# Performance work log

Hardware: AMD Instinct MI355X
Metric: run time of the kernel (lower is better)

Reference implementation:

```python
import jax, jax.numpy as jnp
import numpy as np

HIDDEN = 1024
HEADS = 16
HEAD_DIM = HIDDEN // HEADS
SCALE = HEAD_DIM ** -0.5
NEG_INF = float(-2 ** 32 + 1)


def setup_inputs() -> dict:
    key = jax.random.key(0)
    ks = jax.random.split(key, 10)
    B, N = 8, 1024
    std = HIDDEN ** -0.5
    inp = {
        "query": jax.random.normal(ks[0], (B, N, HIDDEN), dtype=jnp.float32),
        "mask": jax.random.randint(ks[1], (B, N), 0, 2, dtype=jnp.int32),
        "Wq": jax.random.normal(ks[2], (HIDDEN, HIDDEN), dtype=jnp.float32) * std,
        "bq": jnp.zeros((HIDDEN,), dtype=jnp.float32),
        "Wk": jax.random.normal(ks[3], (HIDDEN, HIDDEN), dtype=jnp.float32) * std,
        "bk": jnp.zeros((HIDDEN,), dtype=jnp.float32),
        "Wv": jax.random.normal(ks[4], (HIDDEN, HIDDEN), dtype=jnp.float32) * std,
        "bv": jnp.zeros((HIDDEN,), dtype=jnp.float32),
        "Wo": jax.random.normal(ks[5], (HIDDEN, HIDDEN), dtype=jnp.float32) * std,
        "bo": jnp.zeros((HIDDEN,), dtype=jnp.float32),
    }
    return inp


def reference(query, mask, Wq, bq, Wk, bk, Wv, bv, Wo, bo):
    B, N, C = query.shape
    H, D = HEADS, HEAD_DIM
    # projections: [B,N,C] -> [B,H,N,D]
    q = (query @ Wq + bq).reshape(B, N, H, D).transpose(0, 2, 1, 3)
    k = (query @ Wk + bk).reshape(B, N, H, D).transpose(0, 2, 1, 3)
    v = (query @ Wv + bv).reshape(B, N, H, D).transpose(0, 2, 1, 3)
    # scores [B,H,N,S]
    attn = jnp.einsum("bhnd,bhsd->bhns", q, k) * SCALE
    # padding mask broadcast over query positions: mask [B,S] -> [B,1,1,S]
    m = mask[:, None, None, :]
    attn = jnp.where(m == 0, jnp.float32(NEG_INF), attn)
    attn = jax.nn.softmax(attn, axis=-1)
    out = jnp.einsum("bhns,bhsd->bhnd", attn, v)
    out = out.transpose(0, 2, 1, 3).reshape(B, N, C)
    out = out @ Wo + bo
    return out
```

## Files before the change

### kernel.cpp

```cpp
#include <hip/hip_runtime.h>
#include <hip/hip_bf16.h>

typedef __bf16 bf16x8 __attribute__((ext_vector_type(8)));
typedef float f32x4 __attribute__((ext_vector_type(4)));
typedef float f32x16 __attribute__((ext_vector_type(16)));
typedef int i32x2 __attribute__((ext_vector_type(2)));
typedef __hip_bfloat16 bf16;

#define QK_SCALE 0.1803368801111204f

__device__ __forceinline__ f32x4 mfma_bf16(bf16x8 a, bf16x8 b, f32x4 c) {
  return __builtin_amdgcn_mfma_f32_16x16x32_bf16(a, b, c, 0, 0, 0);
}
__device__ __forceinline__ f32x16 mfma32(bf16x8 a, bf16x8 b, f32x16 c) {
  return __builtin_amdgcn_mfma_f32_32x32x16_bf16(a, b, c, 0, 0, 0);
}

__device__ __forceinline__ void gload16(const void* g, void* l) {
  __builtin_amdgcn_global_load_lds(
      (const __attribute__((address_space(1))) void*)g,
      (__attribute__((address_space(3))) void*)l, 16, 0, 0);
}

__global__ void cvt_bf16_kernel(const float* __restrict__ in, bf16* __restrict__ out) {
  int i = (blockIdx.x * 256 + threadIdx.x) * 4;
  float4 v = *reinterpret_cast<const float4*>(in + i);
  union { bf16 h[4]; uint2 u; } t;
  t.h[0] = __float2bfloat16(v.x);
  t.h[1] = __float2bfloat16(v.y);
  t.h[2] = __float2bfloat16(v.z);
  t.h[3] = __float2bfloat16(v.w);
  *reinterpret_cast<uint2*>(out + i) = t.u;
}

__global__ void transpose_w_kernel(const float* __restrict__ Wq, const float* __restrict__ Wk,
                                   const float* __restrict__ Wv, const float* __restrict__ Wo,
                                   bf16* __restrict__ Wqkv_t, bf16* __restrict__ Wot) {
  __shared__ float tile[32][33];
  int z = blockIdx.z;
  const float* src = (z == 0) ? Wq : (z == 1) ? Wk : (z == 2) ? Wv : Wo;
  bf16* dst = (z < 3) ? (Wqkv_t + (size_t)z * 1048576) : Wot;
  int tx = threadIdx.x, ty = threadIdx.y;
  int c0 = blockIdx.x * 32, r0 = blockIdx.y * 32;
#pragma unroll
  for (int i = 0; i < 32; i += 8)
    tile[ty + i][tx] = src[(r0 + ty + i) * 1024 + c0 + tx];
  __syncthreads();
#pragma unroll
  for (int i = 0; i < 32; i += 8)
    dst[(c0 + ty + i) * 1024 + r0 + tx] = __float2bfloat16(tile[tx][ty + i]);
}

__global__ __launch_bounds__(256) void gemm_qkv_kernel(
    const bf16* __restrict__ A, const bf16* __restrict__ Bt,
    const float* __restrict__ bq, const float* __restrict__ bk, const float* __restrict__ bv,
    bf16* __restrict__ Qb, bf16* __restrict__ Kb, bf16* __restrict__ Vt) {
  __shared__ __align__(16) bf16 As[2][128 * 32];
  __shared__ __align__(16) bf16 Bs[2][128 * 32];
  const int K = 1024;
  const int TILES_N = 24;
  const int NWG = 1536, CPX = NWG / 8;
  int bid0 = blockIdx.x;
  int bid = (bid0 % 8) * CPX + bid0 / 8;
  int bm = bid / TILES_N, bn = bid % TILES_N;
  int t = threadIdx.x;
  int lane = t & 63, w = t >> 6;
  int fr = lane & 15, fk = (lane >> 4) * 8;
  int wr = w >> 1, wc = w & 1;
  int srow = t >> 2, scol = (t & 3) * 8;

  const bf16* Ablk = A + (size_t)(bm * 128) * K;
  const bf16* Bblk = Bt + (size_t)(bn * 128) * K;

  auto stage = [&](int bufi, int k0) {
    char* ad = (char*)As[bufi] + t * 16;
    char* bd = (char*)Bs[bufi] + t * 16;
    gload16(Ablk + (size_t)srow * K + k0 + scol, ad);
    gload16(Ablk + (size_t)(srow + 64) * K + k0 + scol, ad + 4096);
    gload16(Bblk + (size_t)srow * K + k0 + scol, bd);
    gload16(Bblk + (size_t)(srow + 64) * K + k0 + scol, bd + 4096);
  };

  f32x4 acc[4][4] = {};

  stage(0, 0);
  __syncthreads();

  for (int k0 = 0; k0 < K; k0 += 32) {
    int cur = (k0 >> 5) & 1;
    if (k0 + 32 < K) stage(cur ^ 1, k0 + 32);
    bf16x8 a[4], b[4];
#pragma unroll
    for (int m = 0; m < 4; m++) a[m] = *(const bf16x8*)&As[cur][(wr * 64 + m * 16 + fr) * 32 + fk];
#pragma unroll
    for (int n = 0; n < 4; n++) b[n] = *(const bf16x8*)&Bs[cur][(wc * 64 + n * 16 + fr) * 32 + fk];
#pragma unroll
    for (int m = 0; m < 4; m++)
#pragma unroll
      for (int n = 0; n < 4; n++)
        acc[m][n] = mfma_bf16(a[m], b[n], acc[m][n]);
    __syncthreads();
  }

  int sel = (bn * 128) >> 10;
  const float* bias = (sel == 0) ? bq : (sel == 1) ? bk : bv;
#pragma unroll
  for (int m = 0; m < 4; m++) {
#pragma unroll
    for (int n = 0; n < 4; n++) {
      f32x4 c = acc[m][n];
      if (sel == 2) {
        int grow0 = bm * 128 + wr * 64 + m * 16 + (lane >> 4) * 4;
        int gcol = bn * 128 + wc * 64 + n * 16 + fr;
        int cc = gcol & 1023;
        int bb = grow0 >> 10, nr0 = grow0 & 1023;
        int h = cc >> 6, d = cc & 63;
        union { bf16 h4[4]; uint2 u; } o;
#pragma unroll
        for (int j = 0; j < 4; j++) o.h4[j] = __float2bfloat16(c[j] + bias[cc]);
        *(uint2*)&Vt[((size_t)(bb * 16 + h) * 64 + d) * 1024 + nr0] = o.u;
      } else {
#pragma unroll
        for (int j = 0; j < 4; j++) {
          int grow = bm * 128 + wr * 64 + m * 16 + (lane >> 4) * 4 + j;
          int gcol = bn * 128 + wc * 64 + n * 16 + fr;
          int cc = gcol & 1023;
          float val = c[j] + bias[cc];
          int bb = grow >> 10, nr = grow & 1023;
          int h = cc >> 6, d = cc & 63;
          int bh = bb * 16 + h;
          if (sel == 0) {
            Qb[((size_t)bh * 1024 + nr) * 64 + d] = __float2bfloat16(val * QK_SCALE);
          } else {
            Kb[((size_t)bh * 1024 + nr) * 64 + d] = __float2bfloat16(val);
          }
        }
      }
    }
  }
}

__global__ __launch_bounds__(256) void attn_kernel(
    const bf16* __restrict__ Qb, const bf16* __restrict__ Kb, const bf16* __restrict__ Vt,
    const int* __restrict__ mask, bf16* __restrict__ AO) {
  __shared__ unsigned pmw[32][2][8];
  __shared__ __align__(16) bf16 Ks[2][4096];
  __shared__ __align__(16) bf16 Vs[2][4096];

  int bid = blockIdx.x;
  int logical = (bid & 7) * 128 + (bid >> 3);
  int bh = logical >> 3;
  int qt = logical & 7;
  int b = bh >> 4, h = bh & 15;
  int t = threadIdx.x, w = t >> 6, lane = t & 63;
  int ql = lane & 31, hi = lane >> 5, hi8 = hi * 8;

#pragma unroll
  for (int rep = 0; rep < 2; rep++) {
    int idx = t + rep * 256;
    int T = idx >> 4, hh = (idx >> 3) & 1, i = idx & 7;
    int k0 = T * 32 + hh * 4 + 2 * (i & 1) + 8 * (i >> 1);
    unsigned lo = mask[b * 1024 + k0] ? 0xFFFFu : 0u;
    unsigned hg = mask[b * 1024 + k0 + 1] ? 0xFFFF0000u : 0u;
    pmw[T][hh][i] = lo | hg;
  }

  const bf16* Qh = Qb + (size_t)bh * 65536;
  const bf16* Kh = Kb + (size_t)bh * 65536;
  const bf16* Vh = Vt + (size_t)bh * 65536;

  int r0 = t >> 3;
  int sc = (t & 7) ^ (r0 & 7);

  auto stage = [&](int bufi, int kt) {
    char* kd = (char*)Ks[bufi] + t * 16;
    char* vd = (char*)Vs[bufi] + t * 16;
    gload16(Kh + (size_t)(kt + r0) * 64 + sc * 8, kd);
    gload16(Kh + (size_t)(kt + r0 + 32) * 64 + sc * 8, kd + 4096);
    gload16(Vh + (size_t)r0 * 1024 + kt + sc * 8, vd);
    gload16(Vh + (size_t)(r0 + 32) * 1024 + kt + sc * 8, vd + 4096);
  };

  int qn = qt * 128 + w * 32;
  bf16x8 qf[4];
#pragma unroll
  for (int c = 0; c < 4; c++)
    qf[c] = *(const bf16x8*)&Qh[(qn + ql) * 64 + c * 16 + hi8];

  bf16x8 ones;
#pragma unroll
  for (int j = 0; j < 8; j++) ones[j] = (__bf16)1.0f;

  f32x16 accO0 = {}, accO1 = {}, accL = {};
  float mrow = -3.0e38f;

  stage(0, 0);
  __syncthreads();

  for (int kt = 0; kt < 1024; kt += 64) {
    int cur = (kt >> 6) & 1;
    if (kt + 64 < 1024) stage(cur ^ 1, kt + 64);
    const char* Kc = (const char*)Ks[cur];
    const char* Vc = (const char*)Vs[cur];

#pragma unroll
    for (int sub = 0; sub < 2; sub++) {
      int Ti = (kt >> 5) + sub;

      int krow = sub * 32 + ql;
      int ksw = (krow & 7) << 4;
      f32x16 s = {};
#pragma unroll
      for (int c = 0; c < 4; c++) {
        bf16x8 kf = *(const bf16x8*)(Kc + krow * 128 + ((c * 32 + hi * 16) ^ ksw));
        s = mfma32(kf, qf[c], s);
      }

      float m0 = fmaxf(fmaxf(s[0], s[1]), s[2]);
      float m1 = fmaxf(fmaxf(s[3], s[4]), s[5]);
      float m2 = fmaxf(fmaxf(s[6], s[7]), s[8]);
      float m3 = fmaxf(fmaxf(s[9], s[10]), s[11]);
      float m4 = fmaxf(fmaxf(s[12], s[13]), s[14]);
      float pm = fmaxf(fmaxf(fmaxf(m0, m1), m2), fmaxf(fmaxf(m3, m4), s[15]));
      pm = fmaxf(pm, __shfl_xor(pm, 32));

      if (!__all(pm - mrow <= 8.0f)) {
        float mnew = fmaxf(mrow, pm);
        float corr = __builtin_amdgcn_exp2f(mrow - mnew);
        accL[0] *= corr;
#pragma unroll
        for (int r = 0; r < 16; r++) { accO0[r] *= corr; accO1[r] *= corr; }
        mrow = mnew;
      }

#pragma unroll
      for (int r = 0; r < 16; r++) s[r] = __builtin_amdgcn_exp2f(s[r] - mrow);
      uint4 mwa = *(const uint4*)&pmw[Ti][hi][0];
      uint4 mwb = *(const uint4*)&pmw[Ti][hi][4];
      unsigned wds[8];
#pragma unroll
      for (int i = 0; i < 8; i++) {
        union { bf16 q[2]; unsigned u; } pk_;
        pk_.q[0] = __float2bfloat16(s[2 * i]);
        pk_.q[1] = __float2bfloat16(s[2 * i + 1]);
        wds[i] = pk_.u;
      }
      wds[0] &= mwa.x; wds[1] &= mwa.y; wds[2] &= mwa.z; wds[3] &= mwa.w;
      wds[4] &= mwb.x; wds[5] &= mwb.y; wds[6] &= mwb.z; wds[7] &= mwb.w;

      i32x2 r02 = __builtin_amdgcn_permlane32_swap((int)wds[0], (int)wds[2], false, false);
      i32x2 r13 = __builtin_amdgcn_permlane32_swap((int)wds[1], (int)wds[3], false, false);
      i32x2 r46 = __builtin_amdgcn_permlane32_swap((int)wds[4], (int)wds[6], false, false);
      i32x2 r57 = __builtin_amdgcn_permlane32_swap((int)wds[5], (int)wds[7], false, false);
      union { int i[4]; bf16x8 v; } y0, y1;
      y0.i[0] = r02[0]; y0.i[1] = r13[0]; y0.i[2] = r02[1]; y0.i[3] = r13[1];
      y1.i[0] = r46[0]; y1.i[1] = r57[0]; y1.i[2] = r46[1]; y1.i[3] = r57[1];

      int vr0 = ql, vr1 = 32 + ql;
      int vs0 = (vr0 & 7) << 4, vs1 = (vr1 & 7) << 4;
      bf16x8 vc0 = *(const bf16x8*)(Vc + vr0 * 128 + ((sub * 64 + hi * 16) ^ vs0));
      bf16x8 vc1 = *(const bf16x8*)(Vc + vr0 * 128 + ((sub * 64 + 32 + hi * 16) ^ vs0));
      bf16x8 vc2 = *(const bf16x8*)(Vc + vr1 * 128 + ((sub * 64 + hi * 16) ^ vs1));
      bf16x8 vc3 = *(const bf16x8*)(Vc + vr1 * 128 + ((sub * 64 + 32 + hi * 16) ^ vs1));
      accO0 = mfma32(vc0, y0.v, accO0);
      accO0 = mfma32(vc1, y1.v, accO0);
      accO1 = mfma32(vc2, y0.v, accO1);
      accO1 = mfma32(vc3, y1.v, accO1);
      accL = mfma32(ones, y0.v, accL);
      accL = mfma32(ones, y1.v, accL);
    }
    __syncthreads();
  }

  float rl = 1.0f / accL[0];
  size_t rowbase = ((size_t)(b * 1024 + qn + ql)) * 1024 + h * 64;
#pragma unroll
  for (int dt = 0; dt < 2; dt++) {
#pragma unroll
    for (int q = 0; q < 4; q++) {
      union { bf16 h4[4]; uint2 u; } o;
#pragma unroll
      for (int j = 0; j < 4; j++) {
        float a = (dt == 0) ? accO0[4 * q + j] : accO1[4 * q + j];
        o.h4[j] = __float2bfloat16(a * rl);
      }
      *(uint2*)&AO[rowbase + dt * 32 + q * 8 + 4 * hi] = o.u;
    }
  }
}

__global__ __launch_bounds__(256) void gemm_out_kernel(
    const bf16* __restrict__ A, const bf16* __restrict__ Bt,
    const float* __restrict__ bo, float* __restrict__ Out) {
  __shared__ __align__(16) bf16 As[2][128 * 32];
  __shared__ __align__(16) bf16 Bs[2][128 * 32];
  const int K = 1024;
  const int TILES_N = 8;
  const int NWG = 512, CPX = NWG / 8;
  int bid0 = blockIdx.x;
  int bid = (bid0 % 8) * CPX + bid0 / 8;
  int bm = bid / TILES_N, bn = bid % TILES_N;
  int t = threadIdx.x;
  int lane = t & 63, w = t >> 6;
  int fr = lane & 15, fk = (lane >> 4) * 8;
  int wr = w >> 1, wc = w & 1;
  int srow = t >> 2, scol = (t & 3) * 8;

  const bf16* Ablk = A + (size_t)(bm * 128) * K;
  const bf16* Bblk = Bt + (size_t)(bn * 128) * K;

  auto stage = [&](int bufi, int k0) {
    char* ad = (char*)As[bufi] + t * 16;
    char* bd = (char*)Bs[bufi] + t * 16;
    gload16(Ablk + (size_t)srow * K + k0 + scol, ad);
    gload16(Ablk + (size_t)(srow + 64) * K + k0 + scol, ad + 4096);
    gload16(Bblk + (size_t)srow * K + k0 + scol, bd);
    gload16(Bblk + (size_t)(srow + 64) * K + k0 + scol, bd + 4096);
  };

  f32x4 acc[4][4] = {};

  stage(0, 0);
  __syncthreads();

  for (int k0 = 0; k0 < K; k0 += 32) {
    int cur = (k0 >> 5) & 1;
    if (k0 + 32 < K) stage(cur ^ 1, k0 + 32);
    bf16x8 a[4], b[4];
#pragma unroll
    for (int m = 0; m < 4; m++) a[m] = *(const bf16x8*)&As[cur][(wr * 64 + m * 16 + fr) * 32 + fk];
#pragma unroll
    for (int n = 0; n < 4; n++) b[n] = *(const bf16x8*)&Bs[cur][(wc * 64 + n * 16 + fr) * 32 + fk];
#pragma unroll
    for (int m = 0; m < 4; m++)
#pragma unroll
      for (int n = 0; n < 4; n++)
        acc[m][n] = mfma_bf16(a[m], b[n], acc[m][n]);
    __syncthreads();
  }

#pragma unroll
  for (int m = 0; m < 4; m++) {
#pragma unroll
    for (int n = 0; n < 4; n++) {
      f32x4 c = acc[m][n];
#pragma unroll
      for (int j = 0; j < 4; j++) {
        int grow = bm * 128 + wr * 64 + m * 16 + (lane >> 4) * 4 + j;
        int gcol = bn * 128 + wc * 64 + n * 16 + fr;
        Out[(size_t)grow * 1024 + gcol] = c[j] + bo[gcol];
      }
    }
  }
}

extern "C" void kernel_launch(void* const* d_in, const int* in_sizes, int n_in,
                              void* d_out, int out_size, void* d_ws, size_t ws_size,
                              hipStream_t stream) {
  const float* X = (const float*)d_in[0];
  const int* mask = (const int*)d_in[1];
  const float* Wq = (const float*)d_in[2];
  const float* bq = (const float*)d_in[3];
  const float* Wk = (const float*)d_in[4];
  const float* bk = (const float*)d_in[5];
  const float* Wv = (const float*)d_in[6];
  const float* bv = (const float*)d_in[7];
  const float* Wo = (const float*)d_in[8];
  const float* bo = (const float*)d_in[9];
  float* Out = (float*)d_out;

  char* ws = (char*)d_ws;
  bf16* Xb     = (bf16*)(ws + 0);
  bf16* Wqkv_t = (bf16*)(ws + 16777216);
  bf16* Wot    = (bf16*)(ws + 23068672);
  bf16* Qb     = (bf16*)(ws + 25165824);
  bf16* Kb     = (bf16*)(ws + 41943040);
  bf16* Vt     = (bf16*)(ws + 58720256);
  bf16* AO     = Xb;

  cvt_bf16_kernel<<<8192, 256, 0, stream>>>(X, Xb);
  transpose_w_kernel<<<dim3(32, 32, 4), dim3(32, 8), 0, stream>>>(Wq, Wk, Wv, Wo, Wqkv_t, Wot);
  gemm_qkv_kernel<<<1536, 256, 0, stream>>>(Xb, Wqkv_t, bq, bk, bv, Qb, Kb, Vt);
  attn_kernel<<<1024, 256, 0, stream>>>(Qb, Kb, Vt, mask, AO);
  gemm_out_kernel<<<512, 256, 0, stream>>>(AO, Wot, bo, Out);
}
```

Before: 174.6 us.

## Enlarge QKV GEMM tiles to 256x256x64 with swizzled LDS and 512 threads

Rewrites the QKV projection GEMM to use 256x256 output tiles with a K-step of 64, 8 waves per block, and 384 workgroups instead of 1536. The LDS layout is XOR-swizzled to avoid bank conflicts, the inner loop is split into four phases with s_setprio around MFMA bursts, and the prefetch of the next K tile overlaps compute. The aim is higher arithmetic intensity and less global/LDS traffic per FLOP. In exchange it uses 128KB of LDS and more accumulator registers, which lowers occupancy, and 384 blocks may fill the 256 CUs unevenly.

```diff
diff --git a/kernel.cpp b/kernel.cpp
--- a/kernel.cpp
+++ b/kernel.cpp
@@ -51,83 +51,109 @@
     dst[(c0 + ty + i) * 1024 + r0 + tx] = __float2bfloat16(tile[tx][ty + i]);
 }
 
-__global__ __launch_bounds__(256) void gemm_qkv_kernel(
+__global__ __launch_bounds__(512) void gemm_qkv_kernel(
     const bf16* __restrict__ A, const bf16* __restrict__ Bt,
     const float* __restrict__ bq, const float* __restrict__ bk, const float* __restrict__ bv,
     bf16* __restrict__ Qb, bf16* __restrict__ Kb, bf16* __restrict__ Vt) {
-  __shared__ __align__(16) bf16 As[2][128 * 32];
-  __shared__ __align__(16) bf16 Bs[2][128 * 32];
+  __shared__ __align__(16) bf16 As[2][256 * 64];
+  __shared__ __align__(16) bf16 Bs[2][256 * 64];
   const int K = 1024;
-  const int TILES_N = 24;
-  const int NWG = 1536, CPX = NWG / 8;
+  const int TILES_N = 12;
+  const int NWG = 384, CPX = NWG / 8;
   int bid0 = blockIdx.x;
   int bid = (bid0 % 8) * CPX + bid0 / 8;
   int bm = bid / TILES_N, bn = bid % TILES_N;
   int t = threadIdx.x;
   int lane = t & 63, w = t >> 6;
-  int fr = lane & 15, fk = (lane >> 4) * 8;
-  int wr = w >> 1, wc = w & 1;
-  int srow = t >> 2, scol = (t & 3) * 8;
-
-  const bf16* Ablk = A + (size_t)(bm * 128) * K;
-  const bf16* Bblk = Bt + (size_t)(bn * 128) * K;
-
-  auto stage = [&](int bufi, int k0) {
-    char* ad = (char*)As[bufi] + t * 16;
-    char* bd = (char*)Bs[bufi] + t * 16;
-    gload16(Ablk + (size_t)srow * K + k0 + scol, ad);
-    gload16(Ablk + (size_t)(srow + 64) * K + k0 + scol, ad + 4096);
-    gload16(Bblk + (size_t)srow * K + k0 + scol, bd);
-    gload16(Bblk + (size_t)(srow + 64) * K + k0 + scol, bd + 4096);
+  int fr = lane & 15, g4 = lane >> 4;
+  int wm = w >> 2, wn = w & 3;
+  int sr = t >> 3;
+  int scJ = (t & 7) ^ (sr & 7);
+
+  const bf16* Ablk = A + (size_t)(bm * 256) * K;
+  const bf16* Bblk = Bt + (size_t)(bn * 256) * K;
+
+  auto stage = [&](int buf, int k0) {
+#pragma unroll
+    for (int c = 0; c < 4; c++) {
+      gload16(Ablk + (size_t)(c * 64 + sr) * K + k0 + scJ * 8,
+              (char*)As[buf] + c * 8192 + t * 16);
+      gload16(Bblk + (size_t)(c * 64 + sr) * K + k0 + scJ * 8,
+              (char*)Bs[buf] + c * 8192 + t * 16);
+    }
   };
 
-  f32x4 acc[4][4] = {};
+  f32x4 acc[8][4] = {};
 
   stage(0, 0);
-  __syncthreads();
-
-  for (int k0 = 0; k0 < K; k0 += 32) {
-    int cur = (k0 >> 5) & 1;
-    if (k0 + 32 < K) stage(cur ^ 1, k0 + 32);
-    bf16x8 a[4], b[4];
-#pragma unroll
-    for (int m = 0; m < 4; m++) a[m] = *(const bf16x8*)&As[cur][(wr * 64 + m * 16 + fr) * 32 + fk];
-#pragma unroll
-    for (int n = 0; n < 4; n++) b[n] = *(const bf16x8*)&Bs[cur][(wc * 64 + n * 16 + fr) * 32 + fk];
-#pragma unroll
-    for (int m = 0; m < 4; m++)
-#pragma unroll
-      for (int n = 0; n < 4; n++)
-        acc[m][n] = mfma_bf16(a[m], b[n], acc[m][n]);
-    __syncthreads();
-  }
-
-  int sel = (bn * 128) >> 10;
+
+  for (int it = 0; it < 16; it++) {
+    int cur = it & 1;
+    asm volatile("s_waitcnt vmcnt(0)" ::: "memory");
+    __builtin_amdgcn_s_barrier();
+    const char* Ac = (const char*)As[cur];
+    const char* Bc = (const char*)Bs[cur];
+#pragma unroll
+    for (int ph = 0; ph < 4; ph++) {
+      int qm = ph >> 1, qn = ph & 1;
+      if (ph == 0 && it + 1 < 16) stage(cur ^ 1, (it + 1) * 64);
+      bf16x8 af[4][2], bg[2][2];
+#pragma unroll
+      for (int mi = 0; mi < 4; mi++) {
+        int R = wm * 128 + qm * 64 + mi * 16 + fr;
+#pragma unroll
+        for (int ks = 0; ks < 2; ks++) {
+          int cc = ks * 4 + g4;
+          af[mi][ks] = *(const bf16x8*)(Ac + R * 128 + ((cc ^ (R & 7)) * 16));
+        }
+      }
+#pragma unroll
+      for (int ni = 0; ni < 2; ni++) {
+        int R = wn * 64 + qn * 32 + ni * 16 + fr;
+#pragma unroll
+        for (int ks = 0; ks < 2; ks++) {
+          int cc = ks * 4 + g4;
+          bg[ni][ks] = *(const bf16x8*)(Bc + R * 128 + ((cc ^ (R & 7)) * 16));
+        }
+      }
+      __builtin_amdgcn_s_setprio(1);
+#pragma unroll
+      for (int mi = 0; mi < 4; mi++)
+#pragma unroll
+        for (int ni = 0; ni < 2; ni++) {
+          acc[qm * 4 + mi][qn * 2 + ni] =
+              mfma_bf16(af[mi][0], bg[ni][0], acc[qm * 4 + mi][qn * 2 + ni]);
+          acc[qm * 4 + mi][qn * 2 + ni] =
+              mfma_bf16(af[mi][1], bg[ni][1], acc[qm * 4 + mi][qn * 2 + ni]);
+        }
+      __builtin_amdgcn_s_setprio(0);
+      __builtin_amdgcn_s_barrier();
+    }
+  }
+
+  int sel = (bn * 256) >> 10;
   const float* bias = (sel == 0) ? bq : (sel == 1) ? bk : bv;
 #pragma unroll
-  for (int m = 0; m < 4; m++) {
-#pragma unroll
-    for (int n = 0; n < 4; n++) {
-      f32x4 c = acc[m][n];
+  for (int mi = 0; mi < 8; mi++) {
+#pragma unroll
+    for (int ni = 0; ni < 4; ni++) {
+      f32x4 c = acc[mi][ni];
+      int grow0 = bm * 256 + wm * 128 + mi * 16 + g4 * 4;
+      int gcol = bn * 256 + wn * 64 + ni * 16 + fr;
+      int cc2 = gcol & 1023;
+      int bb = grow0 >> 10;
+      int h = cc2 >> 6, d = cc2 & 63;
       if (sel == 2) {
-        int grow0 = bm * 128 + wr * 64 + m * 16 + (lane >> 4) * 4;
-        int gcol = bn * 128 + wc * 64 + n * 16 + fr;
-        int cc = gcol & 1023;
-        int bb = grow0 >> 10, nr0 = grow0 & 1023;
-        int h = cc >> 6, d = cc & 63;
+        int nr0 = grow0 & 1023;
         union { bf16 h4[4]; uint2 u; } o;
 #pragma unroll
-        for (int j = 0; j < 4; j++) o.h4[j] = __float2bfloat16(c[j] + bias[cc]);
+        for (int j = 0; j < 4; j++) o.h4[j] = __float2bfloat16(c[j] + bias[cc2]);
         *(uint2*)&Vt[((size_t)(bb * 16 + h) * 64 + d) * 1024 + nr0] = o.u;
       } else {
 #pragma unroll
         for (int j = 0; j < 4; j++) {
-          int grow = bm * 128 + wr * 64 + m * 16 + (lane >> 4) * 4 + j;
-          int gcol = bn * 128 + wc * 64 + n * 16 + fr;
-          int cc = gcol & 1023;
-          float val = c[j] + bias[cc];
-          int bb = grow >> 10, nr = grow & 1023;
-          int h = cc >> 6, d = cc & 63;
+          int nr = (grow0 + j) & 1023;
+          float val = c[j] + bias[cc2];
           int bh = bb * 16 + h;
           if (sel == 0) {
             Qb[((size_t)bh * 1024 + nr) * 64 + d] = __float2bfloat16(val * QK_SCALE);
@@ -380,7 +406,7 @@
 
   cvt_bf16_kernel<<<8192, 256, 0, stream>>>(X, Xb);
   transpose_w_kernel<<<dim3(32, 32, 4), dim3(32, 8), 0, stream>>>(Wq, Wk, Wv, Wo, Wqkv_t, Wot);
-  gemm_qkv_kernel<<<1536, 256, 0, stream>>>(Xb, Wqkv_t, bq, bk, bv, Qb, Kb, Vt);
+  gemm_qkv_kernel<<<384, 512, 0, stream>>>(Xb, Wqkv_t, bq, bk, bv, Qb, Kb, Vt);
   attn_kernel<<<1024, 256, 0, stream>>>(Qb, Kb, Vt, mask, AO);
   gemm_out_kernel<<<512, 256, 0, stream>>>(AO, Wot, bo, Out);
 }
```

Result: slower. 192.6 us (+10.3%).
